# Optimization experiments

Hardware: AMD Instinct MI355X
Metric: run time of the kernel (lower is better)

Reference implementation:

```python
import jax, jax.numpy as jnp
import numpy as np


def setup_inputs() -> dict:
    key = jax.random.key(0)
    k1, k2, k3 = jax.random.split(key, 3)
    N, K, C, M = 16, 32768, 16, 128
    pred_boxes = jax.random.normal(k1, (N, K, 5), dtype=jnp.float32)
    pred_cls = jax.random.normal(k2, (N, K, C), dtype=jnp.float32)
    target = jax.random.uniform(k3, (N, M, 5), dtype=jnp.float32)
    return {"pred_boxes": pred_boxes, "pred_cls": pred_cls, "target": target}


def _losses(pred_boxes, pred_cls, target):
    N, K, _ = pred_boxes.shape
    M = target.shape[1]
    C = pred_cls.shape[2]
    mask = target.sum(axis=2) != 0                      # (N, M)
    maskf = mask.astype(pred_boxes.dtype)
    denom = maskf.sum()
    tboxes = target[..., 1:]                            # (N, M, 4) corners (x1,y1,x2,y2)
    tcls = target[..., 0].astype(jnp.int32)             # (N, M)
    pconf = pred_boxes[..., 4]                          # (N, K)
    pb = pred_boxes[..., :4]                            # (N, K, 4) (x, y, w, h)

    # pred corners (N, 1, K)
    p_x1 = pb[:, None, :, 0]
    p_y1 = pb[:, None, :, 1]
    p_x2 = (pb[..., 2] + pb[..., 0])[:, None, :]
    p_y2 = (pb[..., 3] + pb[..., 1])[:, None, :]
    # target corners (N, M, 1)
    t_x1 = tboxes[..., 0:1]
    t_y1 = tboxes[..., 1:2]
    t_x2 = tboxes[..., 2:3]
    t_y2 = tboxes[..., 3:4]

    ix1 = jnp.maximum(p_x1, t_x1)
    iy1 = jnp.maximum(p_y1, t_y1)
    ix2 = jnp.minimum(p_x2, t_x2)
    iy2 = jnp.minimum(p_y2, t_y2)
    inter = jnp.clip(ix2 - ix1 + 1, 0) * jnp.clip(iy2 - iy1 + 1, 0)   # (N, M, K)
    a1 = (p_x2 - p_x1 + 1) * (p_y2 - p_y1 + 1)
    a2 = (t_x2 - t_x1 + 1) * (t_y2 - t_y1 + 1)
    iou = inter / (a1 + a2 - inter + 1e-16)

    best = jnp.argmax(iou, axis=-1)                     # (N, M)
    best_idx = jnp.where(mask, best, 0)                 # masked targets keep index 0 (as torch init)

    best_pb = jnp.take_along_axis(pb, best_idx[..., None], axis=1)       # (N, M, 4)
    best_cls = jnp.take_along_axis(pred_cls, best_idx[..., None], axis=1)  # (N, M, C)
    # NOTE: faithful to original: conf gather indices are never updated -> always index 0
    conf_idx = jnp.zeros((N, M), dtype=jnp.int32)
    best_conf = jax.nn.sigmoid(jnp.take_along_axis(pconf, conf_idx, axis=1))  # (N, M)

    def masked_mean(v):
        return (v * maskf).sum() / denom

    logp = jax.nn.log_softmax(best_cls, axis=-1)
    ce = -jnp.take_along_axis(logp, tcls[..., None], axis=-1)[..., 0]
    loss_cls = masked_mean(ce)

    loss_x = masked_mean((best_pb[..., 0] - tboxes[..., 0]) ** 2)
    loss_y = masked_mean((best_pb[..., 1] - tboxes[..., 1]) ** 2)
    loss_w = masked_mean((best_pb[..., 2] - (tboxes[..., 2] - tboxes[..., 0])) ** 2)
    loss_h = masked_mean((best_pb[..., 3] - (tboxes[..., 3] - tboxes[..., 1])) ** 2)

    labels = (best_conf > 0.5).astype(best_conf.dtype)
    bce = -(labels * jnp.log(best_conf) + (1.0 - labels) * jnp.log(1.0 - best_conf))
    loss_conf = masked_mean(bce)

    loss = loss_cls + loss_x + loss_y + loss_w + loss_h + loss_conf
    return loss, loss_cls, loss_x, loss_y, loss_w, loss_h, loss_conf


def reference(pred_boxes, pred_cls, target):
    return _losses(pred_boxes, pred_cls, target)
```

## Files before the change

kernel.cpp:

```cpp
#include <hip/hip_runtime.h>
#include <math.h>

constexpr int N_ = 16;
constexpr int K_ = 32768;
constexpr int C_ = 16;
constexpr int M_ = 128;

constexpr int KC = 256;
constexpr int CHUNKS = K_ / KC;
constexpr int WAVES = 4;
constexpr int GROUPS = 16;

#define POISON_U 0xAAAAAAAAu

__device__ __forceinline__ unsigned long long load_agent_u64(
    const unsigned long long* p) {
  return __hip_atomic_load(p, __ATOMIC_RELAXED, __HIP_MEMORY_SCOPE_AGENT);
}
__device__ __forceinline__ void store_agent_f32(float* p, float v) {
  __hip_atomic_store(p, v, __ATOMIC_RELAXED, __HIP_MEMORY_SCOPE_AGENT);
}
__device__ __forceinline__ float load_agent_f32(const float* p) {
  return __hip_atomic_load(p, __ATOMIC_RELAXED, __HIP_MEMORY_SCOPE_AGENT);
}

__global__ __launch_bounds__(256, 8) void fused_loss_kernel(
    const float* __restrict__ pred_boxes,
    const float* __restrict__ pred_cls,
    const float* __restrict__ target,
    unsigned long long* __restrict__ rowmin,
    float* __restrict__ ws2,
    int* __restrict__ cnt,
    float* __restrict__ out) {
  __shared__ float4 lds4[KC];
  __shared__ float ldsa1[KC];
  __shared__ int key_s[WAVES][M_];
  __shared__ float red[4][7];
  __shared__ int s_flag;

  const int chunk = blockIdx.x;
  const int n = blockIdx.y;
  const int k0 = chunk * KC;
  const int tid = threadIdx.x;

  {
    const float* p = pred_boxes + ((size_t)(n * K_ + k0 + tid)) * 5;
    const float x = p[0];
    const float y = p[1];
    const float bw = p[2];
    const float bh = p[3];
    const float px2 = bw + x;
    const float py2 = bh + y;
    lds4[tid] = make_float4(x, y, px2 + 1.0f, py2 + 1.0f);
    ldsa1[tid] = (px2 - x + 1.0f) * (py2 - y + 1.0f);
  }
  __syncthreads();

  const int wv = tid >> 6;
  const int lane = tid & 63;
  const int rb = lane & 31;
  const int half = (lane >> 5) & 1;
  const int ks = (wv * 2 + half) * 32;
  const int hbase = ((1 - half) << 5) | 31;

  float tx1[4], ty1[4], tx2[4], ty2[4], a2[4];
#pragma unroll
  for (int j = 0; j < 4; ++j) {
    const float* tg = target + ((size_t)(n * M_ + rb + 32 * j)) * 5;
    tx1[j] = tg[1];
    ty1[j] = tg[2];
    tx2[j] = tg[3] + 1.0f;
    ty2[j] = tg[4] + 1.0f;
    a2[j] = (tg[3] - tg[1] + 1.0f) * (tg[4] - tg[2] + 1.0f) + 1e-16f;
  }

  int best[4];
#pragma unroll
  for (int j = 0; j < 4; ++j) best[j] = (int)0x80000000;

#pragma unroll 8
  for (int kl = 0; kl < 32; ++kl) {
    const float4 v = lds4[ks + kl];
    const float a1 = ldsa1[ks + kl];
    const unsigned idx6 = (unsigned)(hbase - kl);
#pragma unroll
    for (int j = 0; j < 4; ++j) {
      float ww = fminf(v.z, tx2[j]) - fmaxf(v.x, tx1[j]);
      float hh = fminf(v.w, ty2[j]) - fmaxf(v.y, ty1[j]);
      ww = fmaxf(ww, 0.0f);
      hh = fmaxf(hh, 0.0f);
      const float inter = ww * hh;
      const float iou = inter * __builtin_amdgcn_rcpf((a1 + a2[j]) - inter);
      const int key = (int)((__float_as_uint(iou) & 0xFFFFFFC0u) | idx6);
      best[j] = best[j] > key ? best[j] : key;
    }
  }

#pragma unroll
  for (int j = 0; j < 4; ++j) {
    const int other = __shfl_xor(best[j], 32, 64);
    best[j] = best[j] > other ? best[j] : other;
  }
  if (lane < 32) {
    const unsigned wvf = (unsigned)(3 - wv) << 6;
#pragma unroll
    for (int j = 0; j < 4; ++j) {
      const unsigned u = (unsigned)best[j];
      key_s[wv][rb + 32 * j] = (int)((u & 0xFFFFFF00u) | wvf | (u & 63u));
    }
  }
  __syncthreads();

  if (tid < M_) {
    int mg = key_s[0][tid];
#pragma unroll
    for (int w2 = 1; w2 < WAVES; ++w2) {
      const int v = key_s[w2][tid];
      mg = mg > v ? mg : v;
    }
    const unsigned e = (unsigned)mg & 255u;
    const int gk = k0 + (255 - (int)e);
    const unsigned tr = (unsigned)mg & 0xFFFFFF00u;
    const unsigned ord = tr ^ (unsigned)(((int)tr >> 31) | 0x80000000);
    const int grp = chunk & (GROUPS - 1);
    atomicMin(&rowmin[((size_t)grp * N_ + n) * M_ + tid],
              ((unsigned long long)(~ord) << 32) | (unsigned)gk);
  }

  __syncthreads();
  if (tid == 0) {
    const unsigned old = (unsigned)atomicAdd(&cnt[n], 1);
    s_flag = (old == POISON_U + (CHUNKS - 1)) || (old == CHUNKS - 1);
  }
  __syncthreads();
  if (!s_flag) return;

  {
    const int m = tid & (M_ - 1);
    float acc[7] = {0, 0, 0, 0, 0, 0, 0};
    if (tid < M_) {
      unsigned long long bestk = ~0ull;
#pragma unroll
      for (int g = 0; g < GROUPS; ++g) {
        const unsigned long long pk =
            load_agent_u64(&rowmin[((size_t)g * N_ + n) * M_ + m]);
        bestk = pk < bestk ? pk : bestk;
      }
      const int bidx0 = (int)(unsigned)bestk;

      const float* tg2 = target + ((size_t)(n * M_ + m)) * 5;
      const float t0 = tg2[0], t1 = tg2[1], t2 = tg2[2], t3 = tg2[3],
                  t4 = tg2[4];
      const float sum5 = t0 + t1 + t2 + t3 + t4;
      const float mk = (sum5 != 0.0f) ? 1.0f : 0.0f;
      const int bidx = (sum5 != 0.0f) ? bidx0 : 0;

      const float* pb = pred_boxes + ((size_t)(n * K_ + bidx)) * 5;
      const float b0 = pb[0], b1 = pb[1], bw = pb[2], bh = pb[3];

      const float4* pc =
          (const float4*)(pred_cls + ((size_t)(n * K_ + bidx)) * C_);
      float vals[C_];
#pragma unroll
      for (int q = 0; q < 4; ++q) {
        const float4 vv = pc[q];
        vals[q * 4 + 0] = vv.x;
        vals[q * 4 + 1] = vv.y;
        vals[q * 4 + 2] = vv.z;
        vals[q * 4 + 3] = vv.w;
      }
      int tcls = (int)t0;
      tcls = tcls < 0 ? 0 : (tcls >= C_ ? C_ - 1 : tcls);
      float mx = -INFINITY;
#pragma unroll
      for (int q = 0; q < C_; ++q) mx = fmaxf(mx, vals[q]);
      float se = 0.0f;
#pragma unroll
      for (int q = 0; q < C_; ++q) se += expf(vals[q] - mx);
      const float ce2 = logf(se) + mx - vals[tcls];

      const float dx = b0 - t1;
      const float dy = b1 - t2;
      const float dw = bw - (t3 - t1);
      const float dh = bh - (t4 - t2);

      const float pcf = pred_boxes[(size_t)n * K_ * 5 + 4];
      const float bc = 1.0f / (1.0f + expf(-pcf));
      const float bce = (bc > 0.5f) ? -logf(bc) : -logf(1.0f - bc);

      acc[0] = mk;
      acc[1] = mk * ce2;
      acc[2] = mk * dx * dx;
      acc[3] = mk * dy * dy;
      acc[4] = mk * dw * dw;
      acc[5] = mk * dh * dh;
      acc[6] = mk * bce;
    }

#pragma unroll
    for (int i = 0; i < 7; ++i) {
      float v = acc[i];
      for (int off = 32; off > 0; off >>= 1) v += __shfl_down(v, off, 64);
      acc[i] = v;
    }
    const int lane2 = tid & 63;
    const int wid = tid >> 6;
    if (lane2 == 0) {
#pragma unroll
      for (int i = 0; i < 7; ++i) red[wid][i] = acc[i];
    }
    __syncthreads();

    if (tid == 0) {
#pragma unroll
      for (int i = 0; i < 7; ++i)
        store_agent_f32(&ws2[n * 8 + i],
                        red[0][i] + red[1][i] + red[2][i] + red[3][i]);
    }
    __syncthreads();
    if (tid == 0) {
      const unsigned old2 = (unsigned)atomicAdd(&cnt[N_], 1);
      s_flag = (old2 == POISON_U + (N_ - 1)) || (old2 == N_ - 1);
    }
    __syncthreads();
  }

  if (s_flag && tid == 0) {
    float s[7] = {0, 0, 0, 0, 0, 0, 0};
    for (int nn = 0; nn < N_; ++nn)
#pragma unroll
      for (int i = 0; i < 7; ++i) s[i] += load_agent_f32(&ws2[nn * 8 + i]);
    const float denom = s[0];
    const float lc = s[1] / denom;
    const float lx = s[2] / denom;
    const float ly = s[3] / denom;
    const float lw = s[4] / denom;
    const float lh = s[5] / denom;
    const float lf = s[6] / denom;
    out[0] = lc + lx + ly + lw + lh + lf;
    out[1] = lc;
    out[2] = lx;
    out[3] = ly;
    out[4] = lw;
    out[5] = lh;
    out[6] = lf;
  }
}

extern "C" void kernel_launch(void* const* d_in, const int* in_sizes, int n_in,
                              void* d_out, int out_size, void* d_ws, size_t ws_size,
                              hipStream_t stream) {
  const float* pred_boxes = (const float*)d_in[0];
  const float* pred_cls = (const float*)d_in[1];
  const float* target = (const float*)d_in[2];
  float* out = (float*)d_out;

  unsigned long long* rowmin = (unsigned long long*)d_ws;
  float* ws2 = (float*)(rowmin + (size_t)GROUPS * N_ * M_);
  int* cnt = (int*)(ws2 + N_ * 8);

  dim3 g(CHUNKS, N_);
  fused_loss_kernel<<<g, 256, 0, stream>>>(pred_boxes, pred_cls, target,
                                           rowmin, ws2, cnt, out);
}
```

Measured before the change: 115.6 us.

## Drop LDS box staging and use per-wave completion signaling for finalize

Each lane now reads its predicted boxes straight from global memory with a float4 load and computes corners and area inline, which removes the LDS staging and its barrier. After the per-row atomicMin, only the two waves that own rows keep running. Each of them signals the per-image counter on its own, without block-wide barriers, and the last wave to arrive does the gather and loss reduction for all 128 targets inside a single wave. This is meant to cut barrier and LDS overhead. In exchange it adds redundant global loads (overlapping unaligned float4 reads with a 5-float stride), and it leans on s_waitcnt for ordering the signal, which is a weaker guarantee than a proper fence.

```diff
diff --git a/kernel.cpp b/kernel.cpp
--- a/kernel.cpp
+++ b/kernel.cpp
@@ -10,6 +10,7 @@
 constexpr int CHUNKS = K_ / KC;
 constexpr int WAVES = 4;
 constexpr int GROUPS = 16;
+constexpr int SIGS_PER_N = 2 * CHUNKS;
 
 #define POISON_U 0xAAAAAAAAu
 
@@ -32,29 +33,12 @@
     float* __restrict__ ws2,
     int* __restrict__ cnt,
     float* __restrict__ out) {
-  __shared__ float4 lds4[KC];
-  __shared__ float ldsa1[KC];
   __shared__ int key_s[WAVES][M_];
-  __shared__ float red[4][7];
-  __shared__ int s_flag;
 
   const int chunk = blockIdx.x;
   const int n = blockIdx.y;
   const int k0 = chunk * KC;
   const int tid = threadIdx.x;
-
-  {
-    const float* p = pred_boxes + ((size_t)(n * K_ + k0 + tid)) * 5;
-    const float x = p[0];
-    const float y = p[1];
-    const float bw = p[2];
-    const float bh = p[3];
-    const float px2 = bw + x;
-    const float py2 = bh + y;
-    lds4[tid] = make_float4(x, y, px2 + 1.0f, py2 + 1.0f);
-    ldsa1[tid] = (px2 - x + 1.0f) * (py2 - y + 1.0f);
-  }
-  __syncthreads();
 
   const int wv = tid >> 6;
   const int lane = tid & 63;
@@ -78,15 +62,23 @@
 #pragma unroll
   for (int j = 0; j < 4; ++j) best[j] = (int)0x80000000;
 
-#pragma unroll 8
+  const float* __restrict__ pbox = pred_boxes + ((size_t)(n * K_ + k0 + ks)) * 5;
+
+#pragma unroll 4
   for (int kl = 0; kl < 32; ++kl) {
-    const float4 v = lds4[ks + kl];
-    const float a1 = ldsa1[ks + kl];
+    const float4 v4 = *(const float4*)(pbox + kl * 5);
+    const float x = v4.x;
+    const float y = v4.y;
+    const float px2 = v4.z + x;
+    const float py2 = v4.w + y;
+    const float x2p = px2 + 1.0f;
+    const float y2p = py2 + 1.0f;
+    const float a1 = (px2 - x + 1.0f) * (py2 - y + 1.0f);
     const unsigned idx6 = (unsigned)(hbase - kl);
 #pragma unroll
     for (int j = 0; j < 4; ++j) {
-      float ww = fminf(v.z, tx2[j]) - fmaxf(v.x, tx1[j]);
-      float hh = fminf(v.w, ty2[j]) - fmaxf(v.y, ty1[j]);
+      float ww = fminf(x2p, tx2[j]) - fmaxf(x, tx1[j]);
+      float hh = fminf(y2p, ty2[j]) - fmaxf(y, ty1[j]);
       ww = fmaxf(ww, 0.0f);
       hh = fmaxf(hh, 0.0f);
       const float inter = ww * hh;
@@ -111,11 +103,14 @@
   }
   __syncthreads();
 
-  if (tid < M_) {
-    int mg = key_s[0][tid];
+  if (wv >= 2) return;
+
+  {
+    const int m = tid;
+    int mg = key_s[0][m];
 #pragma unroll
     for (int w2 = 1; w2 < WAVES; ++w2) {
-      const int v = key_s[w2][tid];
+      const int v = key_s[w2][m];
       mg = mg > v ? mg : v;
     }
     const unsigned e = (unsigned)mg & 255u;
@@ -123,127 +118,111 @@
     const unsigned tr = (unsigned)mg & 0xFFFFFF00u;
     const unsigned ord = tr ^ (unsigned)(((int)tr >> 31) | 0x80000000);
     const int grp = chunk & (GROUPS - 1);
-    atomicMin(&rowmin[((size_t)grp * N_ + n) * M_ + tid],
+    atomicMin(&rowmin[((size_t)grp * N_ + n) * M_ + m],
               ((unsigned long long)(~ord) << 32) | (unsigned)gk);
   }
 
-  __syncthreads();
-  if (tid == 0) {
-    const unsigned old = (unsigned)atomicAdd(&cnt[n], 1);
-    s_flag = (old == POISON_U + (CHUNKS - 1)) || (old == CHUNKS - 1);
-  }
-  __syncthreads();
-  if (!s_flag) return;
-
-  {
-    const int m = tid & (M_ - 1);
-    float acc[7] = {0, 0, 0, 0, 0, 0, 0};
-    if (tid < M_) {
-      unsigned long long bestk = ~0ull;
-#pragma unroll
-      for (int g = 0; g < GROUPS; ++g) {
-        const unsigned long long pk =
-            load_agent_u64(&rowmin[((size_t)g * N_ + n) * M_ + m]);
-        bestk = pk < bestk ? pk : bestk;
-      }
-      const int bidx0 = (int)(unsigned)bestk;
-
-      const float* tg2 = target + ((size_t)(n * M_ + m)) * 5;
-      const float t0 = tg2[0], t1 = tg2[1], t2 = tg2[2], t3 = tg2[3],
-                  t4 = tg2[4];
-      const float sum5 = t0 + t1 + t2 + t3 + t4;
-      const float mk = (sum5 != 0.0f) ? 1.0f : 0.0f;
-      const int bidx = (sum5 != 0.0f) ? bidx0 : 0;
-
-      const float* pb = pred_boxes + ((size_t)(n * K_ + bidx)) * 5;
-      const float b0 = pb[0], b1 = pb[1], bw = pb[2], bh = pb[3];
-
-      const float4* pc =
-          (const float4*)(pred_cls + ((size_t)(n * K_ + bidx)) * C_);
-      float vals[C_];
-#pragma unroll
-      for (int q = 0; q < 4; ++q) {
-        const float4 vv = pc[q];
-        vals[q * 4 + 0] = vv.x;
-        vals[q * 4 + 1] = vv.y;
-        vals[q * 4 + 2] = vv.z;
-        vals[q * 4 + 3] = vv.w;
-      }
-      int tcls = (int)t0;
-      tcls = tcls < 0 ? 0 : (tcls >= C_ ? C_ - 1 : tcls);
-      float mx = -INFINITY;
-#pragma unroll
-      for (int q = 0; q < C_; ++q) mx = fmaxf(mx, vals[q]);
-      float se = 0.0f;
-#pragma unroll
-      for (int q = 0; q < C_; ++q) se += expf(vals[q] - mx);
-      const float ce2 = logf(se) + mx - vals[tcls];
-
-      const float dx = b0 - t1;
-      const float dy = b1 - t2;
-      const float dw = bw - (t3 - t1);
-      const float dh = bh - (t4 - t2);
-
-      const float pcf = pred_boxes[(size_t)n * K_ * 5 + 4];
-      const float bc = 1.0f / (1.0f + expf(-pcf));
-      const float bce = (bc > 0.5f) ? -logf(bc) : -logf(1.0f - bc);
-
-      acc[0] = mk;
-      acc[1] = mk * ce2;
-      acc[2] = mk * dx * dx;
-      acc[3] = mk * dy * dy;
-      acc[4] = mk * dw * dw;
-      acc[5] = mk * dh * dh;
-      acc[6] = mk * bce;
-    }
-
-#pragma unroll
-    for (int i = 0; i < 7; ++i) {
-      float v = acc[i];
-      for (int off = 32; off > 0; off >>= 1) v += __shfl_down(v, off, 64);
-      acc[i] = v;
-    }
-    const int lane2 = tid & 63;
-    const int wid = tid >> 6;
-    if (lane2 == 0) {
-#pragma unroll
-      for (int i = 0; i < 7; ++i) red[wid][i] = acc[i];
-    }
-    __syncthreads();
-
-    if (tid == 0) {
-#pragma unroll
-      for (int i = 0; i < 7; ++i)
-        store_agent_f32(&ws2[n * 8 + i],
-                        red[0][i] + red[1][i] + red[2][i] + red[3][i]);
-    }
-    __syncthreads();
-    if (tid == 0) {
-      const unsigned old2 = (unsigned)atomicAdd(&cnt[N_], 1);
-      s_flag = (old2 == POISON_U + (N_ - 1)) || (old2 == N_ - 1);
-    }
-    __syncthreads();
-  }
-
-  if (s_flag && tid == 0) {
-    float s[7] = {0, 0, 0, 0, 0, 0, 0};
-    for (int nn = 0; nn < N_; ++nn)
-#pragma unroll
-      for (int i = 0; i < 7; ++i) s[i] += load_agent_f32(&ws2[nn * 8 + i]);
-    const float denom = s[0];
-    const float lc = s[1] / denom;
-    const float lx = s[2] / denom;
-    const float ly = s[3] / denom;
-    const float lw = s[4] / denom;
-    const float lh = s[5] / denom;
-    const float lf = s[6] / denom;
-    out[0] = lc + lx + ly + lw + lh + lf;
-    out[1] = lc;
-    out[2] = lx;
-    out[3] = ly;
-    out[4] = lw;
-    out[5] = lh;
-    out[6] = lf;
+  __builtin_amdgcn_s_waitcnt(0);
+  int old = 0;
+  if (lane == 0) old = atomicAdd(&cnt[n], 1);
+  old = __shfl(old, 0, 64);
+  const unsigned uo = (unsigned)old;
+  if (!(uo == POISON_U + (SIGS_PER_N - 1) || uo == SIGS_PER_N - 1)) return;
+
+  float acc[7] = {0, 0, 0, 0, 0, 0, 0};
+#pragma unroll
+  for (int r = 0; r < 2; ++r) {
+    const int m = lane + r * 64;
+    unsigned long long bestk = ~0ull;
+#pragma unroll
+    for (int g = 0; g < GROUPS; ++g) {
+      const unsigned long long pk =
+          load_agent_u64(&rowmin[((size_t)g * N_ + n) * M_ + m]);
+      bestk = pk < bestk ? pk : bestk;
+    }
+    const int bidx0 = (int)(unsigned)bestk;
+
+    const float* tg2 = target + ((size_t)(n * M_ + m)) * 5;
+    const float t0 = tg2[0], t1 = tg2[1], t2 = tg2[2], t3 = tg2[3],
+                t4 = tg2[4];
+    const float sum5 = t0 + t1 + t2 + t3 + t4;
+    const float mk = (sum5 != 0.0f) ? 1.0f : 0.0f;
+    const int bidx = (sum5 != 0.0f) ? bidx0 : 0;
+
+    const float* pb = pred_boxes + ((size_t)(n * K_ + bidx)) * 5;
+    const float b0 = pb[0], b1 = pb[1], bw = pb[2], bh = pb[3];
+
+    const float4* pc =
+        (const float4*)(pred_cls + ((size_t)(n * K_ + bidx)) * C_);
+    float vals[C_];
+#pragma unroll
+    for (int q = 0; q < 4; ++q) {
+      const float4 vv = pc[q];
+      vals[q * 4 + 0] = vv.x;
+      vals[q * 4 + 1] = vv.y;
+      vals[q * 4 + 2] = vv.z;
+      vals[q * 4 + 3] = vv.w;
+    }
+    int tcls = (int)t0;
+    tcls = tcls < 0 ? 0 : (tcls >= C_ ? C_ - 1 : tcls);
+    float mx = -INFINITY;
+#pragma unroll
+    for (int q = 0; q < C_; ++q) mx = fmaxf(mx, vals[q]);
+    float se = 0.0f;
+#pragma unroll
+    for (int q = 0; q < C_; ++q) se += expf(vals[q] - mx);
+    const float ce2 = logf(se) + mx - vals[tcls];
+
+    const float dx = b0 - t1;
+    const float dy = b1 - t2;
+    const float dw = bw - (t3 - t1);
+    const float dh = bh - (t4 - t2);
+
+    const float pcf = pred_boxes[(size_t)n * K_ * 5 + 4];
+    const float bc = 1.0f / (1.0f + expf(-pcf));
+    const float bce = (bc > 0.5f) ? -logf(bc) : -logf(1.0f - bc);
+
+    acc[0] += mk;
+    acc[1] += mk * ce2;
+    acc[2] += mk * dx * dx;
+    acc[3] += mk * dy * dy;
+    acc[4] += mk * dw * dw;
+    acc[5] += mk * dh * dh;
+    acc[6] += mk * bce;
+  }
+
+#pragma unroll
+  for (int i = 0; i < 7; ++i) {
+    float v = acc[i];
+    for (int off = 32; off > 0; off >>= 1) v += __shfl_down(v, off, 64);
+    acc[i] = v;
+  }
+
+  if (lane == 0) {
+#pragma unroll
+    for (int i = 0; i < 7; ++i) store_agent_f32(&ws2[n * 8 + i], acc[i]);
+    __builtin_amdgcn_s_waitcnt(0);
+    const unsigned old2 = (unsigned)atomicAdd(&cnt[N_], 1);
+    if (old2 == POISON_U + (N_ - 1) || old2 == N_ - 1) {
+      float s[7] = {0, 0, 0, 0, 0, 0, 0};
+      for (int nn = 0; nn < N_; ++nn)
+#pragma unroll
+        for (int i = 0; i < 7; ++i) s[i] += load_agent_f32(&ws2[nn * 8 + i]);
+      const float denom = s[0];
+      const float lc = s[1] / denom;
+      const float lx = s[2] / denom;
+      const float ly = s[3] / denom;
+      const float lw = s[4] / denom;
+      const float lh = s[5] / denom;
+      const float lf = s[6] / denom;
+      out[0] = lc + lx + ly + lw + lh + lf;
+      out[1] = lc;
+      out[2] = lx;
+      out[3] = ly;
+      out[4] = lw;
+      out[5] = lh;
+      out[6] = lf;
+    }
   }
 }
 
```

After: 143.9 us. 24.5% more time.
